# Kernel optimization log

Hardware: AMD Instinct MI355X
Metric: run time of the kernel (lower is better)

Reference implementation:

```python
import jax, jax.numpy as jnp
import numpy as np

N, R, E, H, F = 50000, 6, 32768, 256, 16
NH, HD = 8, 32
EPS_LN = 1e-5

def _ln(x, g, b):
    mu = x.mean(-1, keepdims=True)
    var = ((x - mu) ** 2).mean(-1, keepdims=True)
    return (x - mu) * jax.lax.rsqrt(var + EPS_LN) * g + b

def setup_inputs() -> dict:
    key = jax.random.key(0)
    ks = jax.random.split(key, 32)
    s = lambda i, shape, scale=0.05: jax.random.normal(ks[i], shape, jnp.float32) * scale
    return {
        'x': jax.random.normal(ks[0], (N, H), jnp.float32),
        'edge_index': jax.random.randint(ks[1], (R, 2, E), 0, N, jnp.int32),
        'edge_attr': jax.random.normal(ks[2], (R, E, F), jnp.float32),
        'Wq': s(3, (R, H, H)), 'bq': s(4, (R, H)),
        'Wk': s(5, (R, H + F, H)), 'bk': s(6, (R, H)),
        'Wv': s(7, (R, H + F, H)), 'bv': s(8, (R, H)),
        'prior': jnp.ones((R, NH), jnp.float32),
        'Wm': s(9, (R, H, H)), 'bm': s(10, (R, H)),
        'W_ir1': s(11, (R * H, H)), 'b_ir1': s(12, (H,)),
        'W_ir2': s(13, (H, R)), 'b_ir2': s(14, (R,)),
        'Wmp': s(15, (3, H, H)), 'bmp': s(16, (3, H)),
        'Wa1': s(17, (H, H // 2)), 'ba1': s(18, (H // 2,)),
        'Wa2': s(19, (H // 2, 1)),
        'g_meta': jnp.ones((H,), jnp.float32), 'b_meta': jnp.zeros((H,), jnp.float32),
        'Wc': s(20, (2 * H, H)), 'bc': s(21, (H,)),
        'g_out': jnp.ones((H,), jnp.float32), 'b_out': jnp.zeros((H,), jnp.float32),
    }

def _block(x, edge_index, edge_attr, Wq, bq, Wk, bk, Wv, bv, prior, Wm, bm,
           W_ir1, b_ir1, W_ir2, b_ir2, Wmp, bmp, Wa1, ba1, Wa2, g_meta, b_meta,
           Wc, bc, g_out, b_out):
    def rel_layer(eidx, eattr, wq, bq_, wk, bk_, wv, bv_, pr, wm, bm_):
        src, dst = eidx[0], eidx[1]
        q = x @ wq + bq_                                  # [N,H]
        kv_in = jnp.concatenate([x[src], eattr], -1)      # [E,H+F]
        k = (kv_in @ wk + bk_).reshape(E, NH, HD)
        v = (kv_in @ wv + bv_).reshape(E, NH, HD)
        qe = q[dst].reshape(E, NH, HD)
        scores = (qe * k).sum(-1) / np.sqrt(HD) * pr      # [E,NH]
        m = jax.ops.segment_max(scores, dst, num_segments=N)
        ex = jnp.exp(scores - m[dst])
        denom = jax.ops.segment_sum(ex, dst, num_segments=N)
        w = ex / (denom[dst] + 1e-16)
        wv_flat = (w[..., None] * v).reshape(E, H)
        agg = jax.ops.segment_sum(wv_flat, dst, num_segments=N)  # [N,H]
        return jax.nn.gelu(agg @ wm + bm_, approximate=False)

    rel_out = jax.vmap(rel_layer)(edge_index, edge_attr, Wq, bq, Wk, bk, Wv, bv,
                                  prior, Wm, bm)          # [R,N,H]

    all_rel = jnp.transpose(rel_out, (1, 0, 2)).reshape(N, R * H)
    h = jax.nn.gelu(all_rel @ W_ir1 + b_ir1, approximate=False)
    inter_w = jax.nn.softmax(h @ W_ir2 + b_ir2, axis=-1)  # [N,R]
    inter_agg = jnp.einsum('nr,rnh->nh', inter_w, rel_out)

    # meta-paths: 0=entangle(ENTANGLE=2,SWAP=3) 1=control(CONTROL=4,ROTATION=0) 2=local(PAULI=1,TEMPORAL=5)
    paths = jnp.stack([rel_out[2] + rel_out[3], rel_out[4] + rel_out[0],
                       rel_out[1] + rel_out[5]], axis=1)  # [N,3,H]
    stacked = jnp.einsum('nph,phk->npk', paths, Wmp) + bmp
    attn = jax.nn.softmax((jnp.tanh(stacked @ Wa1 + ba1) @ Wa2).squeeze(-1), axis=1)
    meta = _ln((attn[..., None] * stacked).sum(1), g_meta, b_meta)

    combined = jax.nn.gelu(jnp.concatenate([inter_agg, meta], -1) @ Wc + bc,
                           approximate=False)
    return _ln(x + combined, g_out, b_out)

def reference(x, edge_index, edge_attr, Wq, bq, Wk, bk, Wv, bv, prior, Wm, bm,
              W_ir1, b_ir1, W_ir2, b_ir2, Wmp, bmp, Wa1, ba1, Wa2, g_meta, b_meta,
              Wc, bc, g_out, b_out):
    return _block(x, edge_index, edge_attr, Wq, bq, Wk, bk, Wv, bv, prior, Wm, bm,
                  W_ir1, b_ir1, W_ir2, b_ir2, Wmp, bmp, Wa1, ba1, Wa2,
                  g_meta, b_meta, Wc, bc, g_out, b_out)
```

## Files before the change

kernel.cpp:

```cpp
#include <hip/hip_runtime.h>
#include <hip/hip_bf16.h>

typedef __hip_bfloat16 bf16;
typedef __attribute__((ext_vector_type(8))) short short8;
typedef __attribute__((ext_vector_type(4))) float f32x4;

#define NN 50000
#define RR 6
#define EE 32768
#define HH 256
#define FF 16
#define NHEAD 8
#define KVP 288

struct __align__(8) bf16x4 { bf16 v[4]; };

__device__ __forceinline__ float b2f(bf16 v) { return __bfloat162float(v); }
__device__ __forceinline__ bf16 f2b(float v) { return __float2bfloat16(v); }
__device__ __forceinline__ short f2s(float f) { bf16 b = f2b(f); return __builtin_bit_cast(short, b); }
__device__ __forceinline__ float s2f(short s) { return b2f(__builtin_bit_cast(bf16, s)); }
__device__ __forceinline__ float gelu_f(float x) { return 0.5f * x * (1.0f + erff(x * 0.7071067811865476f)); }
__device__ __forceinline__ unsigned fkey(float f) { unsigned u = __float_as_uint(f); return (u & 0x80000000u) ? ~u : (u | 0x80000000u); }
__device__ __forceinline__ float fdec(unsigned k) { unsigned u = (k & 0x80000000u) ? (k & 0x7fffffffu) : ~k; return __uint_as_float(u); }

__device__ __forceinline__ void gl2lds16(const void* g, void* l) {
  __builtin_amdgcn_global_load_lds(
      (const __attribute__((address_space(1))) unsigned int*)g,
      (__attribute__((address_space(3))) unsigned int*)l, 16, 0, 0);
}

__global__ void zero_k(uint4* __restrict__ p, int n16)
{
  const uint4 z = make_uint4(0u, 0u, 0u, 0u);
  for (int i = blockIdx.x * blockDim.x + threadIdx.x; i < n16; i += gridDim.x * blockDim.x)
    p[i] = z;
}

__global__ void tconv_k(const float* __restrict__ in, bf16* __restrict__ out,
                        int K, int NC, int Kp, long izs, long ozs)
{
  __shared__ float t[32][33];
  in  += (size_t)blockIdx.z * izs;
  out += (size_t)blockIdx.z * ozs;
  const int kb = blockIdx.x * 32, nb = blockIdx.y * 32;
  const int tx = threadIdx.x & 31, ty = threadIdx.x >> 5;
  for (int i = ty; i < 32; i += 8) {
    const int k = kb + i, n = nb + tx;
    t[i][tx] = (k < K && n < NC) ? in[(size_t)k * NC + n] : 0.f;
  }
  __syncthreads();
  for (int i = ty; i < 32; i += 8) {
    const int n = nb + i, k = kb + tx;
    if (n < NC && k < Kp) out[(size_t)n * Kp + k] = f2b(t[tx][i]);
  }
}

__global__ void bkv_k(const float* __restrict__ bk, const float* __restrict__ bv,
                      float* __restrict__ bkv)
{
  const int i = blockIdx.x * 256 + threadIdx.x;
  if (i >= RR * 512) return;
  const int r = i >> 9, c = i & 511;
  bkv[i] = (c < 256) ? bk[r * 256 + c] : bv[r * 256 + (c - 256)];
}

__global__ void copyslot_k(const bf16* __restrict__ tmp, bf16* __restrict__ slot)
{
  const int i = blockIdx.x * 256 + threadIdx.x;
  if (i >= NN * 32) return;
  const int n = i >> 5, c = (i & 31) * 8;
  *(short8*)(slot + (size_t)n * 1536 + c) = *(const short8*)(tmp + (size_t)n * 256 + c);
}

template<int ASRC, int ACT, bool LOGITS, typename TO>
__global__ __launch_bounds__(256) void mm_k(
    const void* __restrict__ Av, const bf16* __restrict__ A2, int lda,
    const int* __restrict__ src, const float* __restrict__ eattr,
    const bf16* __restrict__ Bt, const float* __restrict__ bias,
    const float* __restrict__ wa2, TO* __restrict__ C, int ldc,
    float* __restrict__ logits, int M, int K)
{
  __shared__ short lA[128 * 32];
  __shared__ short lB[128 * 32];
  const int tid = threadIdx.x;
  const int w = tid >> 6, l = tid & 63;
  const int row0 = blockIdx.x << 7;
  const int col0 = blockIdx.y << 7;
  const int wm = (w >> 1) << 6, wn = (w & 1) << 6;
  const int lane15 = l & 15, kq = l >> 4;

  f32x4 acc[4][4] = {};

  for (int k0 = 0; k0 < K; k0 += 32) {
#pragma unroll
    for (int i = 0; i < 2; ++i) {
      const int idx = (w * 2 + i) * 64 + l;
      const int row = idx >> 2, cg = idx & 3;
      const int r = min(row0 + row, M - 1);
      const int kc = k0 + cg * 8;
      if constexpr (ASRC == 0) {
        gl2lds16((const bf16*)Av + (size_t)r * lda + kc, &lA[idx * 8]);
      } else if constexpr (ASRC == 1) {
        const float* p = (const float*)Av + (size_t)r * lda + kc;
        const float4 f0 = *(const float4*)p;
        const float4 f1 = *(const float4*)(p + 4);
        short8 s;
        s[0] = f2s(f0.x); s[1] = f2s(f0.y); s[2] = f2s(f0.z); s[3] = f2s(f0.w);
        s[4] = f2s(f1.x); s[5] = f2s(f1.y); s[6] = f2s(f1.z); s[7] = f2s(f1.w);
        *(short8*)&lA[idx * 8] = s;
      } else if constexpr (ASRC == 2) {
        const short8 u = *(const short8*)((const bf16*)Av + (size_t)r * lda + kc);
        const short8 v2 = *(const short8*)(A2 + (size_t)r * lda + kc);
        short8 s;
#pragma unroll
        for (int j = 0; j < 8; ++j) s[j] = f2s(s2f(u[j]) + s2f(v2[j]));
        *(short8*)&lA[idx * 8] = s;
      } else {
        short8 s;
        if (kc < HH) {
          const float* p = (const float*)Av + (size_t)src[r] * HH + kc;
          const float4 f0 = *(const float4*)p;
          const float4 f1 = *(const float4*)(p + 4);
          s[0] = f2s(f0.x); s[1] = f2s(f0.y); s[2] = f2s(f0.z); s[3] = f2s(f0.w);
          s[4] = f2s(f1.x); s[5] = f2s(f1.y); s[6] = f2s(f1.z); s[7] = f2s(f1.w);
        } else if (kc < HH + FF) {
          const float* p = eattr + (size_t)r * FF + (kc - HH);
          const float4 f0 = *(const float4*)p;
          const float4 f1 = *(const float4*)(p + 4);
          s[0] = f2s(f0.x); s[1] = f2s(f0.y); s[2] = f2s(f0.z); s[3] = f2s(f0.w);
          s[4] = f2s(f1.x); s[5] = f2s(f1.y); s[6] = f2s(f1.z); s[7] = f2s(f1.w);
        } else {
#pragma unroll
          for (int j = 0; j < 8; ++j) s[j] = 0;
        }
        *(short8*)&lA[idx * 8] = s;
      }
    }
#pragma unroll
    for (int i = 0; i < 2; ++i) {
      const int idx = (w * 2 + i) * 64 + l;
      const int row = idx >> 2, cg = idx & 3;
      gl2lds16(Bt + (size_t)(col0 + row) * K + k0 + cg * 8, &lB[idx * 8]);
    }
    __syncthreads();
    short8 af[4], bfr[4];
#pragma unroll
    for (int t = 0; t < 4; ++t) {
      af[t]  = *(const short8*)&lA[(wm + t * 16 + lane15) * 32 + kq * 8];
      bfr[t] = *(const short8*)&lB[(wn + t * 16 + lane15) * 32 + kq * 8];
    }
#pragma unroll
    for (int ti = 0; ti < 4; ++ti)
#pragma unroll
      for (int tj = 0; tj < 4; ++tj)
        acc[ti][tj] = __builtin_amdgcn_mfma_f32_16x16x32_bf16(af[ti], bfr[tj], acc[ti][tj], 0, 0, 0);
    __syncthreads();
  }

  if constexpr (!LOGITS) {
#pragma unroll
    for (int ti = 0; ti < 4; ++ti) {
#pragma unroll
      for (int reg = 0; reg < 4; ++reg) {
        const int row = row0 + wm + ti * 16 + kq * 4 + reg;
        if (row >= M) continue;
#pragma unroll
        for (int tj = 0; tj < 4; ++tj) {
          const int col = col0 + wn + tj * 16 + lane15;
          float v = acc[ti][tj][reg] + bias[col];
          if constexpr (ACT == 1) v = gelu_f(v);
          if constexpr (sizeof(TO) == 2) C[(size_t)row * ldc + col] = (TO)f2b(v);
          else                           C[(size_t)row * ldc + col] = (TO)v;
        }
      }
    }
  } else {
#pragma unroll
    for (int ti = 0; ti < 4; ++ti) {
#pragma unroll
      for (int reg = 0; reg < 4; ++reg) {
        float part = 0.f;
#pragma unroll
        for (int tj = 0; tj < 4; ++tj) {
          const int col = col0 + wn + tj * 16 + lane15;
          part += tanhf(acc[ti][tj][reg] + bias[col]) * wa2[col];
        }
#pragma unroll
        for (int off = 8; off > 0; off >>= 1) part += __shfl_xor(part, off, 64);
        const int row = row0 + wm + ti * 16 + kq * 4 + reg;
        if (lane15 == 0 && row < M) atomicAdd(&logits[row], part);
      }
    }
  }
}

__global__ void scores_k(const bf16* __restrict__ q, const bf16* __restrict__ kv,
                         const int* __restrict__ dst_idx, const float* __restrict__ prior_r,
                         float* __restrict__ scores, unsigned* __restrict__ mkey)
{
  const int e = blockIdx.x, t = threadIdx.x;
  const int dst = dst_idx[e];
  float p = b2f(q[(size_t)dst * 1536 + t]) * b2f(kv[(size_t)e * 512 + t]);
#pragma unroll
  for (int off = 16; off > 0; off >>= 1) p += __shfl_down(p, off, 32);
  const int h = t >> 5;
  if ((t & 31) == 0) {
    const float s = p * 0.1767766952966369f * prior_r[h];
    scores[e * NHEAD + h] = s;
    atomicMax(&mkey[dst * NHEAD + h], fkey(s));
  }
}

__global__ void expden_k(const float* __restrict__ scores, const int* __restrict__ dst_idx,
                         const unsigned* __restrict__ mkey, float* __restrict__ ex,
                         float* __restrict__ denom)
{
  const int idx = blockIdx.x * 256 + threadIdx.x;
  if (idx >= EE * NHEAD) return;
  const int e = idx >> 3, h = idx & 7;
  const int dst = dst_idx[e];
  const float m = fdec(mkey[dst * NHEAD + h]);
  const float v = expf(scores[idx] - m);
  ex[idx] = v;
  atomicAdd(&denom[dst * NHEAD + h], v);
}

__global__ void agg_k(const float* __restrict__ ex, const float* __restrict__ denom,
                      const bf16* __restrict__ kv, const int* __restrict__ dst_idx,
                      float* __restrict__ agg)
{
  const int e = blockIdx.x, t = threadIdx.x, h = t >> 5;
  const int dst = dst_idx[e];
  const float w = ex[e * NHEAD + h] / (denom[dst * NHEAD + h] + 1e-16f);
  atomicAdd(&agg[(size_t)dst * HH + t], w * b2f(kv[(size_t)e * 512 + 256 + t]));
}

__global__ void interw_k(const bf16* __restrict__ h, const float* __restrict__ W2,
                         const float* __restrict__ b2, float* __restrict__ interw)
{
  const int wv = threadIdx.x >> 6, ln = threadIdx.x & 63;
  const int n = blockIdx.x * 4 + wv;
  if (n >= NN) return;
  float a[6] = {0.f, 0.f, 0.f, 0.f, 0.f, 0.f};
#pragma unroll
  for (int kq = 0; kq < 4; ++kq) {
    const int k = ln + (kq << 6);
    const float hv = b2f(h[(size_t)n * HH + k]);
#pragma unroll
    for (int j = 0; j < 6; ++j) a[j] += hv * W2[k * 6 + j];
  }
#pragma unroll
  for (int j = 0; j < 6; ++j) {
#pragma unroll
    for (int off = 32; off > 0; off >>= 1) a[j] += __shfl_down(a[j], off, 64);
  }
  if (ln == 0) {
    float lg[6], e[6], mx = -1e30f, s = 0.f;
#pragma unroll
    for (int j = 0; j < 6; ++j) { lg[j] = a[j] + b2[j]; mx = fmaxf(mx, lg[j]); }
#pragma unroll
    for (int j = 0; j < 6; ++j) { e[j] = expf(lg[j] - mx); s += e[j]; }
    const float inv = 1.0f / s;
#pragma unroll
    for (int j = 0; j < 6; ++j) interw[(size_t)n * 6 + j] = e[j] * inv;
  }
}

__global__ void interagg_k(const float* __restrict__ interw, const bf16* __restrict__ rel_cat,
                           bf16* __restrict__ comb)
{
  const int n = blockIdx.x, t = threadIdx.x;
  float acc = 0.f;
#pragma unroll
  for (int r = 0; r < 6; ++r)
    acc += interw[(size_t)n * 6 + r] * b2f(rel_cat[(size_t)n * 1536 + r * 256 + t]);
  comb[(size_t)n * 512 + t] = f2b(acc);
}

__global__ void metafinal_k(const float* __restrict__ logits, const bf16* __restrict__ rel_cat,
                            const float* __restrict__ gmeta, const float* __restrict__ bmeta,
                            bf16* __restrict__ comb)
{
  const int wv = threadIdx.x >> 6, ln = threadIdx.x & 63;
  const int n = blockIdx.x * 4 + wv;
  if (n >= NN) return;
  const float l0 = logits[n], l1 = logits[NN + n], l2 = logits[2 * NN + n];
  const float mx = fmaxf(l0, fmaxf(l1, l2));
  const float e0 = expf(l0 - mx), e1 = expf(l1 - mx), e2 = expf(l2 - mx);
  const float inv = 1.0f / (e0 + e1 + e2);
  const float a0 = e0 * inv, a1 = e1 * inv, a2 = e2 * inv;
  const size_t base = (size_t)n * 1536;
  float pre[4], s = 0.f, s2 = 0.f;
#pragma unroll
  for (int q4 = 0; q4 < 4; ++q4) {
    const int j = ln + (q4 << 6);
    const float v = a0 * b2f(rel_cat[base + 2 * 256 + j])
                  + a1 * b2f(rel_cat[base + 4 * 256 + j])
                  + a2 * b2f(rel_cat[base + 1 * 256 + j]);
    pre[q4] = v; s += v; s2 += v * v;
  }
#pragma unroll
  for (int off = 32; off > 0; off >>= 1) { s += __shfl_down(s, off, 64); s2 += __shfl_down(s2, off, 64); }
  s = __shfl(s, 0, 64); s2 = __shfl(s2, 0, 64);
  const float mu = s * (1.0f / 256.0f);
  const float var = s2 * (1.0f / 256.0f) - mu * mu;
  const float rs = rsqrtf(var + 1e-5f);
#pragma unroll
  for (int q4 = 0; q4 < 4; ++q4) {
    const int j = ln + (q4 << 6);
    comb[(size_t)n * 512 + 256 + j] = f2b((pre[q4] - mu) * rs * gmeta[j] + bmeta[j]);
  }
}

__global__ void final_k(const float* __restrict__ x, const float* __restrict__ combined,
                        const float* __restrict__ g, const float* __restrict__ b,
                        float* __restrict__ out)
{
  __shared__ float sred[8];
  const int n = blockIdx.x, t = threadIdx.x;
  const float v = x[(size_t)n * HH + t] + combined[(size_t)n * HH + t];
  float s = v, s2 = v * v;
#pragma unroll
  for (int off = 32; off > 0; off >>= 1) { s += __shfl_down(s, off, 64); s2 += __shfl_down(s2, off, 64); }
  const int wv = t >> 6;
  if ((t & 63) == 0) { sred[wv] = s; sred[4 + wv] = s2; }
  __syncthreads();
  const float st = sred[0] + sred[1] + sred[2] + sred[3];
  const float st2 = sred[4] + sred[5] + sred[6] + sred[7];
  const float mu = st * (1.0f / 256.0f);
  const float var = st2 * (1.0f / 256.0f) - mu * mu;
  const float rs = rsqrtf(var + 1e-5f);
  out[(size_t)n * HH + t] = (v - mu) * rs * g[t] + b[t];
}

extern "C" void kernel_launch(void* const* d_in, const int* in_sizes, int n_in,
                              void* d_out, int out_size, void* d_ws, size_t ws_size,
                              hipStream_t stream)
{
  const float* x      = (const float*)d_in[0];
  const int*   eidx   = (const int*)d_in[1];
  const float* eattr  = (const float*)d_in[2];
  const float* Wq     = (const float*)d_in[3];
  const float* bq     = (const float*)d_in[4];
  const float* Wk     = (const float*)d_in[5];
  const float* bk     = (const float*)d_in[6];
  const float* Wv     = (const float*)d_in[7];
  const float* bv     = (const float*)d_in[8];
  const float* prior  = (const float*)d_in[9];
  const float* Wm     = (const float*)d_in[10];
  const float* bm     = (const float*)d_in[11];
  const float* W_ir1  = (const float*)d_in[12];
  const float* b_ir1  = (const float*)d_in[13];
  const float* W_ir2  = (const float*)d_in[14];
  const float* b_ir2  = (const float*)d_in[15];
  const float* Wmp    = (const float*)d_in[16];
  const float* bmp    = (const float*)d_in[17];
  const float* Wa1    = (const float*)d_in[18];
  const float* ba1    = (const float*)d_in[19];
  const float* Wa2    = (const float*)d_in[20];
  const float* g_meta = (const float*)d_in[21];
  const float* b_meta = (const float*)d_in[22];
  const float* Wc     = (const float*)d_in[23];
  const float* bc     = (const float*)d_in[24];
  const float* g_out  = (const float*)d_in[25];
  const float* b_out  = (const float*)d_in[26];
  float* out = (float*)d_out;

  char* ws = (char*)d_ws;
  bf16* rel_cat = (bf16*)ws;
  char* W0 = ws + 153600000;
  bf16*  Wqt   = (bf16*)(W0 + 0);
  bf16*  Wkvt  = (bf16*)(W0 + 786432);
  bf16*  Wmt   = (bf16*)(W0 + 2555904);
  bf16*  Wir1t = (bf16*)(W0 + 3342336);
  bf16*  Wct   = (bf16*)(W0 + 4128768);
  bf16*  Wmpt  = (bf16*)(W0 + 4390912);
  bf16*  Wa1t  = (bf16*)(W0 + 4784128);
  float* bkv   = (float*)(W0 + 4849664);
  char* region = ws + 158461952;
  bf16*     kvbuf = (bf16*)(region + 0);
  float*    sc    = (float*)(region + 59154432);
  float*    exb   = (float*)(region + 60203008);
  unsigned* mkey  = (unsigned*)(region + 61251584);
  float*    denom = (float*)(region + 62851584);
  float*    agg   = out;
  bf16*  hbuf     = (bf16*)(region + 0);
  float* interw   = (float*)(region + 59154432);
  bf16*  tmp      = (bf16*)(region + 25600000);
  float* logits   = (float*)(region + 61251584);
  bf16*  comb     = (bf16*)out;
  float* combined = (float*)(region + 0);

  const dim3 gN(391, 2);
  const dim3 gQ(391, 12);
  const dim3 gKV(256, 4);
  const dim3 gL(391, 1);

  tconv_k<<<dim3(8, 8, 6), 256, 0, stream>>>(Wq, Wqt, 256, 256, 256, 256 * 256, 256 * 256);
  tconv_k<<<dim3(9, 8, 6), 256, 0, stream>>>(Wk, Wkvt, 272, 256, 288, 272 * 256, 512 * 288);
  tconv_k<<<dim3(9, 8, 6), 256, 0, stream>>>(Wv, Wkvt + 256 * 288, 272, 256, 288, 272 * 256, 512 * 288);
  tconv_k<<<dim3(8, 8, 6), 256, 0, stream>>>(Wm, Wmt, 256, 256, 256, 256 * 256, 256 * 256);
  tconv_k<<<dim3(48, 8, 1), 256, 0, stream>>>(W_ir1, Wir1t, 1536, 256, 1536, 0, 0);
  tconv_k<<<dim3(16, 8, 1), 256, 0, stream>>>(Wc, Wct, 512, 256, 512, 0, 0);
  tconv_k<<<dim3(8, 8, 3), 256, 0, stream>>>(Wmp, Wmpt, 256, 256, 256, 256 * 256, 256 * 256);
  tconv_k<<<dim3(8, 4, 1), 256, 0, stream>>>(Wa1, Wa1t, 256, 128, 256, 0, 0);
  bkv_k<<<12, 256, 0, stream>>>(bk, bv, bkv);

  mm_k<1, 0, false, bf16><<<gQ, 256, 0, stream>>>(
      x, nullptr, 256, nullptr, nullptr,
      Wqt, bq, nullptr, rel_cat, 1536, nullptr, NN, 256);

  for (int r = 0; r < RR; ++r) {
    const int* src = eidx + (size_t)r * 2 * EE;
    const int* dst = src + EE;
    const float* ea = eattr + (size_t)r * EE * FF;
    zero_k<<<391, 256, 0, stream>>>((uint4*)mkey, (2 * NN * NHEAD * 4) / 16);
    zero_k<<<2048, 256, 0, stream>>>((uint4*)agg, (NN * HH * 4) / 16);
    mm_k<3, 0, false, bf16><<<gKV, 256, 0, stream>>>(
        x, nullptr, 0, src, ea,
        Wkvt + (size_t)r * 512 * KVP, bkv + r * 512, nullptr, kvbuf, 512, nullptr, EE, KVP);
    scores_k<<<EE, 256, 0, stream>>>(rel_cat + r * 256, kvbuf, dst, prior + r * NHEAD, sc, mkey);
    expden_k<<<(EE * NHEAD + 255) / 256, 256, 0, stream>>>(sc, dst, mkey, exb, denom);
    agg_k<<<EE, 256, 0, stream>>>(exb, denom, kvbuf, dst, agg);
    mm_k<1, 1, false, bf16><<<gN, 256, 0, stream>>>(
        agg, nullptr, 256, nullptr, nullptr,
        Wmt + (size_t)r * 256 * 256, bm + r * HH, nullptr,
        rel_cat + r * 256, 1536, nullptr, NN, 256);
  }

  mm_k<0, 1, false, bf16><<<gN, 256, 0, stream>>>(
      rel_cat, nullptr, 1536, nullptr, nullptr,
      Wir1t, b_ir1, nullptr, hbuf, 256, nullptr, NN, 1536);
  interw_k<<<(NN + 3) / 4, 256, 0, stream>>>(hbuf, W_ir2, b_ir2, interw);
  interagg_k<<<NN, 256, 0, stream>>>(interw, rel_cat, comb);

  const int r1[3] = {2, 4, 1};
  const int r2[3] = {3, 0, 5};
  zero_k<<<147, 256, 0, stream>>>((uint4*)logits, (3 * NN * 4) / 16);
  for (int p = 0; p < 3; ++p) {
    mm_k<2, 0, false, bf16><<<gN, 256, 0, stream>>>(
        rel_cat + r1[p] * 256, rel_cat + r2[p] * 256, 1536, nullptr, nullptr,
        Wmpt + (size_t)p * 256 * 256, bmp + p * 256, nullptr, tmp, 256, nullptr, NN, 256);
    mm_k<0, 0, true, bf16><<<gL, 256, 0, stream>>>(
        tmp, nullptr, 256, nullptr, nullptr,
        Wa1t, ba1, Wa2, (bf16*)nullptr, 0, logits + (size_t)p * NN, NN, 256);
    copyslot_k<<<(NN * 32 + 255) / 256, 256, 0, stream>>>(tmp, rel_cat + r1[p] * 256);
  }
  metafinal_k<<<(NN + 3) / 4, 256, 0, stream>>>(logits, rel_cat, g_meta, b_meta, comb);

  mm_k<0, 1, false, float><<<gN, 256, 0, stream>>>(
      comb, nullptr, 512, nullptr, nullptr,
      Wct, bc, nullptr, combined, 256, nullptr, NN, 512);
  final_k<<<NN, 256, 0, stream>>>(x, combined, g_out, b_out, out);
}
```

Baseline: 1.778 ms.

## Widen GEMM K-tile to 64 with XOR-swizzled LDS and bf16 x precast

The shared GEMM kernel now stages 64-wide K slices with an XOR swizzle on LDS columns, which halves barrier count per K and is meant to avoid LDS bank conflicts. The grid is transposed so column tiles vary fastest, which may improve L2 reuse of A rows. x is converted once to bf16 so the Q GEMM and the gathered KV GEMM read half the bytes; KV padding grows to 320 so the K loop divides by 64, adding some wasted MFMA work. The three per-path logits GEMMs are merged into one launch over blockIdx.z that reads the stored slots in rel_cat.

```diff
diff --git a/kernel.cpp b/kernel.cpp
--- a/kernel.cpp
+++ b/kernel.cpp
@@ -11,7 +11,7 @@
 #define HH 256
 #define FF 16
 #define NHEAD 8
-#define KVP 288
+#define KVP 320
 
 struct __align__(8) bf16x4 { bf16 v[4]; };
 
@@ -34,6 +34,15 @@
   const uint4 z = make_uint4(0u, 0u, 0u, 0u);
   for (int i = blockIdx.x * blockDim.x + threadIdx.x; i < n16; i += gridDim.x * blockDim.x)
     p[i] = z;
+}
+
+__global__ void cvt_k(const float* __restrict__ in, bf16* __restrict__ out, int n4)
+{
+  const int i = blockIdx.x * 256 + threadIdx.x;
+  if (i >= n4) return;
+  const float4 f = ((const float4*)in)[i];
+  bf16x4 o; o.v[0] = f2b(f.x); o.v[1] = f2b(f.y); o.v[2] = f2b(f.z); o.v[3] = f2b(f.w);
+  ((bf16x4*)out)[i] = o;
 }
 
 __global__ void tconv_k(const float* __restrict__ in, bf16* __restrict__ out,
@@ -80,26 +89,34 @@
     const float* __restrict__ wa2, TO* __restrict__ C, int ldc,
     float* __restrict__ logits, int M, int K)
 {
-  __shared__ short lA[128 * 32];
-  __shared__ short lB[128 * 32];
+  __shared__ short lA[128 * 64];
+  __shared__ short lB[128 * 64];
   const int tid = threadIdx.x;
   const int w = tid >> 6, l = tid & 63;
-  const int row0 = blockIdx.x << 7;
-  const int col0 = blockIdx.y << 7;
+  const int col0 = blockIdx.x << 7;
+  const int row0 = blockIdx.y << 7;
+  const bf16* Ab = (const bf16*)Av;
+  float* lg = logits;
+  if constexpr (LOGITS) {
+    const int slots3[3] = {2, 4, 1};
+    Ab = (const bf16*)Av + slots3[blockIdx.z] * 256;
+    lg = logits + (size_t)blockIdx.z * M;
+  }
   const int wm = (w >> 1) << 6, wn = (w & 1) << 6;
   const int lane15 = l & 15, kq = l >> 4;
 
   f32x4 acc[4][4] = {};
 
-  for (int k0 = 0; k0 < K; k0 += 32) {
-#pragma unroll
-    for (int i = 0; i < 2; ++i) {
-      const int idx = (w * 2 + i) * 64 + l;
-      const int row = idx >> 2, cg = idx & 3;
+  for (int k0 = 0; k0 < K; k0 += 64) {
+#pragma unroll
+    for (int i = 0; i < 4; ++i) {
+      const int idx = (w * 4 + i) * 64 + l;
+      const int row = idx >> 3, cg = idx & 7;
+      const int scg = cg ^ (row & 7);
       const int r = min(row0 + row, M - 1);
-      const int kc = k0 + cg * 8;
+      const int kc = k0 + scg * 8;
       if constexpr (ASRC == 0) {
-        gl2lds16((const bf16*)Av + (size_t)r * lda + kc, &lA[idx * 8]);
+        gl2lds16(Ab + (size_t)r * lda + kc, &lA[idx * 8]);
       } else if constexpr (ASRC == 1) {
         const float* p = (const float*)Av + (size_t)r * lda + kc;
         const float4 f0 = *(const float4*)p;
@@ -118,11 +135,7 @@
       } else {
         short8 s;
         if (kc < HH) {
-          const float* p = (const float*)Av + (size_t)src[r] * HH + kc;
-          const float4 f0 = *(const float4*)p;
-          const float4 f1 = *(const float4*)(p + 4);
-          s[0] = f2s(f0.x); s[1] = f2s(f0.y); s[2] = f2s(f0.z); s[3] = f2s(f0.w);
-          s[4] = f2s(f1.x); s[5] = f2s(f1.y); s[6] = f2s(f1.z); s[7] = f2s(f1.w);
+          s = *(const short8*)((const bf16*)Av + (size_t)src[r] * HH + kc);
         } else if (kc < HH + FF) {
           const float* p = eattr + (size_t)r * FF + (kc - HH);
           const float4 f0 = *(const float4*)p;
@@ -137,23 +150,31 @@
       }
     }
 #pragma unroll
-    for (int i = 0; i < 2; ++i) {
-      const int idx = (w * 2 + i) * 64 + l;
-      const int row = idx >> 2, cg = idx & 3;
-      gl2lds16(Bt + (size_t)(col0 + row) * K + k0 + cg * 8, &lB[idx * 8]);
+    for (int i = 0; i < 4; ++i) {
+      const int idx = (w * 4 + i) * 64 + l;
+      const int row = idx >> 3, cg = idx & 7;
+      const int scg = cg ^ (row & 7);
+      gl2lds16(Bt + (size_t)(col0 + row) * K + k0 + scg * 8, &lB[idx * 8]);
     }
     __syncthreads();
-    short8 af[4], bfr[4];
-#pragma unroll
-    for (int t = 0; t < 4; ++t) {
-      af[t]  = *(const short8*)&lA[(wm + t * 16 + lane15) * 32 + kq * 8];
-      bfr[t] = *(const short8*)&lB[(wn + t * 16 + lane15) * 32 + kq * 8];
+#pragma unroll
+    for (int kk = 0; kk < 64; kk += 32) {
+      short8 af[4], bfr[4];
+#pragma unroll
+      for (int t = 0; t < 4; ++t) {
+        const int ra = wm + t * 16 + lane15;
+        const int ca = ((kk >> 3) + kq) ^ (ra & 7);
+        af[t] = *(const short8*)&lA[ra * 64 + ca * 8];
+        const int rb = wn + t * 16 + lane15;
+        const int cb = ((kk >> 3) + kq) ^ (rb & 7);
+        bfr[t] = *(const short8*)&lB[rb * 64 + cb * 8];
+      }
+#pragma unroll
+      for (int ti = 0; ti < 4; ++ti)
+#pragma unroll
+        for (int tj = 0; tj < 4; ++tj)
+          acc[ti][tj] = __builtin_amdgcn_mfma_f32_16x16x32_bf16(af[ti], bfr[tj], acc[ti][tj], 0, 0, 0);
     }
-#pragma unroll
-    for (int ti = 0; ti < 4; ++ti)
-#pragma unroll
-      for (int tj = 0; tj < 4; ++tj)
-        acc[ti][tj] = __builtin_amdgcn_mfma_f32_16x16x32_bf16(af[ti], bfr[tj], acc[ti][tj], 0, 0, 0);
     __syncthreads();
   }
 
@@ -188,7 +209,7 @@
 #pragma unroll
         for (int off = 8; off > 0; off >>= 1) part += __shfl_xor(part, off, 64);
         const int row = row0 + wm + ti * 16 + kq * 4 + reg;
-        if (lane15 == 0 && row < M) atomicAdd(&logits[row], part);
+        if (lane15 == 0 && row < M) atomicAdd(&lg[row], part);
       }
     }
   }
@@ -371,43 +392,45 @@
   char* W0 = ws + 153600000;
   bf16*  Wqt   = (bf16*)(W0 + 0);
   bf16*  Wkvt  = (bf16*)(W0 + 786432);
-  bf16*  Wmt   = (bf16*)(W0 + 2555904);
-  bf16*  Wir1t = (bf16*)(W0 + 3342336);
-  bf16*  Wct   = (bf16*)(W0 + 4128768);
-  bf16*  Wmpt  = (bf16*)(W0 + 4390912);
-  bf16*  Wa1t  = (bf16*)(W0 + 4784128);
-  float* bkv   = (float*)(W0 + 4849664);
-  char* region = ws + 158461952;
+  bf16*  Wmt   = (bf16*)(W0 + 2752512);
+  bf16*  Wir1t = (bf16*)(W0 + 3538944);
+  bf16*  Wct   = (bf16*)(W0 + 4325376);
+  bf16*  Wmpt  = (bf16*)(W0 + 4587520);
+  bf16*  Wa1t  = (bf16*)(W0 + 4980736);
+  float* bkv   = (float*)(W0 + 5046272);
+  char* region = ws + 158658560;
   bf16*     kvbuf = (bf16*)(region + 0);
-  float*    sc    = (float*)(region + 59154432);
-  float*    exb   = (float*)(region + 60203008);
-  unsigned* mkey  = (unsigned*)(region + 61251584);
-  float*    denom = (float*)(region + 62851584);
+  float*    sc    = (float*)(region + 33554432);
+  float*    exb   = (float*)(region + 34603008);
+  unsigned* mkey  = (unsigned*)(region + 35651584);
+  float*    denom = (float*)(region + 37251584);
+  bf16*     xb    = (bf16*)(region + 38851584);
   float*    agg   = out;
   bf16*  hbuf     = (bf16*)(region + 0);
-  float* interw   = (float*)(region + 59154432);
+  float* interw   = (float*)(region + 33554432);
   bf16*  tmp      = (bf16*)(region + 25600000);
-  float* logits   = (float*)(region + 61251584);
+  float* logits   = (float*)(region + 51200000);
   bf16*  comb     = (bf16*)out;
   float* combined = (float*)(region + 0);
 
-  const dim3 gN(391, 2);
-  const dim3 gQ(391, 12);
-  const dim3 gKV(256, 4);
-  const dim3 gL(391, 1);
+  const dim3 gN(2, 391);
+  const dim3 gQ(12, 391);
+  const dim3 gKV(4, 256);
+  const dim3 gL(1, 391, 3);
 
   tconv_k<<<dim3(8, 8, 6), 256, 0, stream>>>(Wq, Wqt, 256, 256, 256, 256 * 256, 256 * 256);
-  tconv_k<<<dim3(9, 8, 6), 256, 0, stream>>>(Wk, Wkvt, 272, 256, 288, 272 * 256, 512 * 288);
-  tconv_k<<<dim3(9, 8, 6), 256, 0, stream>>>(Wv, Wkvt + 256 * 288, 272, 256, 288, 272 * 256, 512 * 288);
+  tconv_k<<<dim3(10, 8, 6), 256, 0, stream>>>(Wk, Wkvt, 272, 256, 320, 272 * 256, 512 * 320);
+  tconv_k<<<dim3(10, 8, 6), 256, 0, stream>>>(Wv, Wkvt + 256 * 320, 272, 256, 320, 272 * 256, 512 * 320);
   tconv_k<<<dim3(8, 8, 6), 256, 0, stream>>>(Wm, Wmt, 256, 256, 256, 256 * 256, 256 * 256);
   tconv_k<<<dim3(48, 8, 1), 256, 0, stream>>>(W_ir1, Wir1t, 1536, 256, 1536, 0, 0);
   tconv_k<<<dim3(16, 8, 1), 256, 0, stream>>>(Wc, Wct, 512, 256, 512, 0, 0);
   tconv_k<<<dim3(8, 8, 3), 256, 0, stream>>>(Wmp, Wmpt, 256, 256, 256, 256 * 256, 256 * 256);
   tconv_k<<<dim3(8, 4, 1), 256, 0, stream>>>(Wa1, Wa1t, 256, 128, 256, 0, 0);
   bkv_k<<<12, 256, 0, stream>>>(bk, bv, bkv);
-
-  mm_k<1, 0, false, bf16><<<gQ, 256, 0, stream>>>(
-      x, nullptr, 256, nullptr, nullptr,
+  cvt_k<<<(NN * 64 + 255) / 256, 256, 0, stream>>>(x, xb, NN * 64);
+
+  mm_k<0, 0, false, bf16><<<gQ, 256, 0, stream>>>(
+      xb, nullptr, 256, nullptr, nullptr,
       Wqt, bq, nullptr, rel_cat, 1536, nullptr, NN, 256);
 
   for (int r = 0; r < RR; ++r) {
@@ -417,7 +440,7 @@
     zero_k<<<391, 256, 0, stream>>>((uint4*)mkey, (2 * NN * NHEAD * 4) / 16);
     zero_k<<<2048, 256, 0, stream>>>((uint4*)agg, (NN * HH * 4) / 16);
     mm_k<3, 0, false, bf16><<<gKV, 256, 0, stream>>>(
-        x, nullptr, 0, src, ea,
+        xb, nullptr, 0, src, ea,
         Wkvt + (size_t)r * 512 * KVP, bkv + r * 512, nullptr, kvbuf, 512, nullptr, EE, KVP);
     scores_k<<<EE, 256, 0, stream>>>(rel_cat + r * 256, kvbuf, dst, prior + r * NHEAD, sc, mkey);
     expden_k<<<(EE * NHEAD + 255) / 256, 256, 0, stream>>>(sc, dst, mkey, exb, denom);
@@ -436,16 +459,16 @@
 
   const int r1[3] = {2, 4, 1};
   const int r2[3] = {3, 0, 5};
-  zero_k<<<147, 256, 0, stream>>>((uint4*)logits, (3 * NN * 4) / 16);
   for (int p = 0; p < 3; ++p) {
     mm_k<2, 0, false, bf16><<<gN, 256, 0, stream>>>(
         rel_cat + r1[p] * 256, rel_cat + r2[p] * 256, 1536, nullptr, nullptr,
         Wmpt + (size_t)p * 256 * 256, bmp + p * 256, nullptr, tmp, 256, nullptr, NN, 256);
-    mm_k<0, 0, true, bf16><<<gL, 256, 0, stream>>>(
-        tmp, nullptr, 256, nullptr, nullptr,
-        Wa1t, ba1, Wa2, (bf16*)nullptr, 0, logits + (size_t)p * NN, NN, 256);
     copyslot_k<<<(NN * 32 + 255) / 256, 256, 0, stream>>>(tmp, rel_cat + r1[p] * 256);
   }
+  zero_k<<<147, 256, 0, stream>>>((uint4*)logits, (3 * NN * 4) / 16);
+  mm_k<0, 0, true, bf16><<<gL, 256, 0, stream>>>(
+      rel_cat, nullptr, 1536, nullptr, nullptr,
+      Wa1t, ba1, Wa2, (bf16*)nullptr, 0, logits, NN, 256);
   metafinal_k<<<(NN + 3) / 4, 256, 0, stream>>>(logits, rel_cat, g_meta, b_meta, comb);
 
   mm_k<0, 1, false, float><<<gN, 256, 0, stream>>>(
```

After: 1.584 ms. 1.12x faster.
